# Performance work log

Hardware: AMD Instinct MI355X
Metric: run time of the kernel (lower is better)

## Reference

```python
import jax, jax.numpy as jnp
import numpy as np

TEMP = 1.0
EPS = 1e-15

B, N, F, K = 8, 2000, 128, 64


def setup_inputs() -> dict:
    key = jax.random.key(0)
    k1, k2, k3 = jax.random.split(key, 3)
    x = jax.random.normal(k1, (B, N, F), dtype=jnp.float32)
    adj = jax.random.uniform(k2, (B, N, N), dtype=jnp.float32)
    s = jax.random.normal(k3, (B, N, K), dtype=jnp.float32)
    mask = jnp.ones((B, N), dtype=bool)
    return {"x": x, "adj": adj, "s": s, "mask": mask}


def reference(x, adj, s, mask):
    k = s.shape[-1]
    s = jax.nn.softmax(s / TEMP, axis=-1)
    m = mask[..., None].astype(x.dtype)          # [B,N,1]
    x = x * m
    s = s * m

    # pooled features: s^T x -> [B,K,F]
    out = jnp.einsum('bnk,bnf->bkf', s, x)

    # pooled adjacency: s^T A s -> [B,K,K]
    as_ = jnp.einsum('bnm,bmk->bnk', adj, s)     # A s, [B,N,K]
    out_adj = jnp.einsum('bnk,bnl->bkl', as_, s)

    # mincut loss
    mincut_num = jnp.einsum('bkk->b', out_adj)
    d_flat = jnp.sum(adj, axis=-1)               # degree, [B,N]
    # trace(s^T diag(d) s) = sum_n d_n * sum_k s_nk^2 (avoids dense diag)
    mincut_den = jnp.einsum('bn,bnk,bnk->b', d_flat, s, s)
    mincut_loss = jnp.mean(-(mincut_num / mincut_den))

    # orthogonality loss
    ss = jnp.einsum('bnk,bnl->bkl', s, s)        # [B,K,K]
    ss_norm = jnp.linalg.norm(ss, axis=(-2, -1), keepdims=True)
    i_s = jnp.eye(k, dtype=ss.dtype)
    ortho = jnp.linalg.norm(ss / ss_norm - i_s / jnp.sqrt(jnp.asarray(k, ss.dtype)), axis=(-2, -1))
    ortho_loss = jnp.mean(ortho)

    # zero diagonal, symmetric degree normalization
    ind = jnp.arange(k)
    out_adj = out_adj.at[:, ind, ind].set(0.0)
    d = jnp.sqrt(jnp.sum(out_adj, axis=-1))[:, None, :] + EPS  # [B,1,K]
    out_adj = out_adj / d / jnp.swapaxes(d, 1, 2)

    return out, out_adj, mincut_loss, ortho_loss
```

## Files before the change

kernel.cpp:

```cpp
#include <hip/hip_runtime.h>

typedef __bf16 bf16;
typedef __bf16 bf16x4 __attribute__((ext_vector_type(4)));
typedef __bf16 bf16x8 __attribute__((ext_vector_type(8)));
typedef float f32x4 __attribute__((ext_vector_type(4)));

#define NB 8
#define NN 2000
#define N2 2048
#define KK 64
#define FF 128

__global__ __launch_bounds__(256) void k1_softmax(const float* __restrict__ s,
                                                  bf16* __restrict__ sT,
                                                  float* __restrict__ rowsq) {
  const int b = blockIdx.x >> 5, tile = blockIdx.x & 31;
  const int n0 = tile * 64;
  const int t = threadIdx.x;
  const int r = t >> 2, q = t & 3;
  __shared__ float ptile[64][65];
  const int n = n0 + r;
  const bool valid = n < NN;
  float v[16];
  if (valid) {
    const float4* src = (const float4*)(s + ((size_t)(b * NN + n)) * KK + q * 16);
#pragma unroll
    for (int i = 0; i < 4; ++i) {
      float4 f = src[i];
      v[4 * i + 0] = f.x; v[4 * i + 1] = f.y; v[4 * i + 2] = f.z; v[4 * i + 3] = f.w;
    }
  } else {
#pragma unroll
    for (int i = 0; i < 16; ++i) v[i] = 0.f;
  }
  float mx = v[0];
#pragma unroll
  for (int i = 1; i < 16; ++i) mx = fmaxf(mx, v[i]);
  mx = fmaxf(mx, __shfl_xor(mx, 1));
  mx = fmaxf(mx, __shfl_xor(mx, 2));
  float sum = 0.f;
#pragma unroll
  for (int i = 0; i < 16; ++i) { v[i] = __expf(v[i] - mx); sum += v[i]; }
  sum += __shfl_xor(sum, 1);
  sum += __shfl_xor(sum, 2);
  const float scale = valid ? (1.0f / sum) : 0.f;
  float rq = 0.f;
#pragma unroll
  for (int i = 0; i < 16; ++i) { v[i] *= scale; rq += v[i] * v[i]; }
  rq += __shfl_xor(rq, 1);
  rq += __shfl_xor(rq, 2);
  if (q == 0) rowsq[b * N2 + n0 + r] = rq;
#pragma unroll
  for (int i = 0; i < 16; ++i) ptile[r][q * 16 + i] = v[i];
  __syncthreads();
  bf16x8 o0, o1;
#pragma unroll
  for (int i = 0; i < 8; ++i) o0[i] = (bf16)ptile[q * 16 + i][r];
#pragma unroll
  for (int i = 0; i < 8; ++i) o1[i] = (bf16)ptile[q * 16 + 8 + i][r];
  bf16* dst = sT + ((size_t)(b * KK + r)) * N2 + n0 + q * 16;
  *(bf16x8*)dst = o0;
  *(bf16x8*)(dst + 8) = o1;
}

__global__ __launch_bounds__(256) void k2_fused(const float* __restrict__ adj,
                                                const bf16* __restrict__ sT,
                                                const float* __restrict__ x,
                                                bf16* __restrict__ xT,
                                                bf16* __restrict__ asT,
                                                const float* __restrict__ rowsq,
                                                float* __restrict__ den_part) {
  __shared__ __align__(16) float smf[64 * 132];
  const int bid = blockIdx.x;
  const int t = threadIdx.x;

  if (bid >= 1024) {
    float* xt = smf;
    const int bb = (bid - 1024) >> 5, tl = (bid - 1024) & 31;
    const int n0b = tl * 64;
#pragma unroll
    for (int i = 0; i < 8; ++i) {
      int idx = t + 256 * i;
      int row = idx >> 5, c4 = idx & 31;
      int n = n0b + row;
      float4 vv = make_float4(0.f, 0.f, 0.f, 0.f);
      if (n < NN) vv = ((const float4*)(x + ((size_t)(bb * NN + n)) * FF))[c4];
      *(float4*)&xt[row * 132 + c4 * 4] = vv;
    }
    __syncthreads();
    const int f = t >> 1, h = t & 1;
    bf16* dst = xT + ((size_t)(bb * FF + f)) * N2 + n0b + h * 32;
#pragma unroll
    for (int g = 0; g < 4; ++g) {
      bf16x8 o;
#pragma unroll
      for (int i = 0; i < 8; ++i) o[i] = (bf16)xt[(h * 32 + g * 8 + i) * 132 + f];
      *(bf16x8*)(dst + g * 8) = o;
    }
    return;
  }

  const int b = bid >> 7, tile = bid & 127;
  if (tile >= 125) {
    if (tile == 125) {
      const int k = t >> 2, seg = t & 3;
      bf16x4 z = {(bf16)0.f, (bf16)0.f, (bf16)0.f, (bf16)0.f};
      bf16* p = asT + ((size_t)(b * KK + k)) * N2 + 2000 + seg * 12;
      *(bf16x4*)(p + 0) = z; *(bf16x4*)(p + 4) = z; *(bf16x4*)(p + 8) = z;
      if (t < 3) den_part[b * 128 + 125 + t] = 0.f;
    }
    return;
  }

  const int w = t >> 6, l = t & 63;
  const int lr = l & 15, lg = l >> 4;
  const int n0 = tile * 16;
  float* dred = smf + 8192;

  const float* adjb = adj + ((size_t)(b * NN + n0)) * NN;
  const bf16* sTw = sT + ((size_t)(b * KK + w * 16 + lr)) * N2;
  const int x7 = lr & 7;

  f32x4 acc;
#pragma unroll
  for (int r = 0; r < 4; ++r) acc[r] = 0.f;

#pragma unroll
  for (int i = 0; i < 4; ++i) {
    const int rr = (w << 2) + i;
    int colf = (l ^ (rr & 7)) << 2;
    if (colf > 1996) colf = 1996;
    __builtin_amdgcn_global_load_lds(adjb + (size_t)rr * NN + colf,
                                     &smf[rr * 256], 16, 0, 0);
  }

  for (int c = 0; c < 8; ++c) {
    __syncthreads();
    if (c < 7) {
      const int nb = (c + 1) & 1;
#pragma unroll
      for (int i = 0; i < 4; ++i) {
        const int rr = (w << 2) + i;
        int colf = (c + 1) * 256 + ((l ^ (rr & 7)) << 2);
        if (colf > 1996) colf = 1996;
        __builtin_amdgcn_global_load_lds(adjb + (size_t)rr * NN + colf,
                                         &smf[nb * 4096 + rr * 256], 16, 0, 0);
      }
    }
    const float* bufc = smf + (c & 1) * 4096 + lr * 256;
    const bf16* sTc = sTw + c * 256;
#pragma unroll
    for (int st = 0; st < 8; ++st) {
      bf16x8 bfrag = *(const bf16x8*)(sTc + st * 32 + lg * 8);
      const int g0 = st * 8 + lg * 2;
      f32x4 a0 = *(const f32x4*)(bufc + ((g0 ^ x7) << 2));
      f32x4 a1 = *(const f32x4*)(bufc + (((g0 + 1) ^ x7) << 2));
      bf16x8 af;
      af[0] = (bf16)a0[0]; af[1] = (bf16)a0[1]; af[2] = (bf16)a0[2]; af[3] = (bf16)a0[3];
      af[4] = (bf16)a1[0]; af[5] = (bf16)a1[1]; af[6] = (bf16)a1[2]; af[7] = (bf16)a1[3];
      acc = __builtin_amdgcn_mfma_f32_16x16x32_bf16(af, bfrag, acc, 0, 0, 0);
    }
  }

  bf16x4 o;
#pragma unroll
  for (int r = 0; r < 4; ++r) o[r] = (bf16)acc[r];
  *(bf16x4*)(asT + ((size_t)(b * KK + w * 16 + lr)) * N2 + n0 + lg * 4) = o;

  float s0 = acc[0], s1 = acc[1], s2 = acc[2], s3 = acc[3];
#pragma unroll
  for (int off = 1; off <= 8; off <<= 1) {
    s0 += __shfl_xor(s0, off); s1 += __shfl_xor(s1, off);
    s2 += __shfl_xor(s2, off); s3 += __shfl_xor(s3, off);
  }
  const float* rqp = rowsq + b * N2 + n0 + lg * 4;
  float part = s0 * rqp[0] + s1 * rqp[1] + s2 * rqp[2] + s3 * rqp[3];
  part += __shfl_xor(part, 16);
  part += __shfl_xor(part, 32);
  if (l == 0) dred[w] = part;
  __syncthreads();
  if (t == 0) den_part[b * 128 + tile] = dred[0] + dred[1] + dred[2] + dred[3];
}

__global__ __launch_bounds__(256) void k3_gemms(const bf16* __restrict__ sT,
                                                const bf16* __restrict__ asT,
                                                const bf16* __restrict__ xT,
                                                float* __restrict__ adjraw,
                                                float* __restrict__ ssw,
                                                float* __restrict__ dout) {
  const int b = blockIdx.x >> 6, u = blockIdx.x & 63;
  const bf16 *Ab, *Bb;
  float* Cb;
  int ldC;
  if (u < 16) {
    const int rt = u >> 2, ct = u & 3;
    Ab = asT + ((size_t)(b * KK + rt * 16)) * N2;
    Bb = sT + ((size_t)(b * KK + ct * 16)) * N2;
    Cb = adjraw + b * KK * KK + rt * 16 * KK + ct * 16; ldC = KK;
  } else if (u < 32) {
    const int v = u - 16, rt = v >> 2, ct = v & 3;
    Ab = sT + ((size_t)(b * KK + rt * 16)) * N2;
    Bb = sT + ((size_t)(b * KK + ct * 16)) * N2;
    Cb = ssw + b * KK * KK + rt * 16 * KK + ct * 16; ldC = KK;
  } else {
    const int v = u - 32, rt = v >> 3, ct = v & 7;
    Ab = sT + ((size_t)(b * KK + rt * 16)) * N2;
    Bb = xT + ((size_t)(b * FF + ct * 16)) * N2;
    Cb = dout + b * KK * FF + rt * 16 * FF + ct * 16; ldC = FF;
  }
  const int t = threadIdx.x;
  const int w = t >> 6, l = t & 63;
  const int lr = l & 15, lg = l >> 4;
  f32x4 acc;
#pragma unroll
  for (int r = 0; r < 4; ++r) acc[r] = 0.f;
  const int m_begin = w * 512;
#pragma unroll 4
  for (int s = 0; s < 16; ++s) {
    const int m = m_begin + s * 32 + lg * 8;
    bf16x8 af = *(const bf16x8*)(Ab + (size_t)lr * N2 + m);
    bf16x8 bfv = *(const bf16x8*)(Bb + (size_t)lr * N2 + m);
    acc = __builtin_amdgcn_mfma_f32_16x16x32_bf16(af, bfv, acc, 0, 0, 0);
  }
  __shared__ float red[4][16][16];
#pragma unroll
  for (int r = 0; r < 4; ++r) red[w][lg * 4 + r][lr] = acc[r];
  __syncthreads();
  const int row = t >> 4, col = t & 15;
  const float v = red[0][row][col] + red[1][row][col] +
                  red[2][row][col] + red[3][row][col];
  Cb[row * ldC + col] = v;
}

__device__ inline float wred64(float v) {
#pragma unroll
  for (int off = 32; off > 0; off >>= 1) v += __shfl_xor(v, off);
  return v;
}

__global__ __launch_bounds__(64) void k4_final(const float* __restrict__ adjraw,
                                               const float* __restrict__ ssw,
                                               const float* __restrict__ den_part,
                                               float* __restrict__ dout,
                                               float* __restrict__ loss_part) {
  const int b = blockIdx.x;
  const int lane = threadIdx.x;
  const float dp = den_part[b * 128 + lane] + den_part[b * 128 + 64 + lane];
  const float den = wred64(dp);
  const float* arow = adjraw + b * 4096 + lane * 64;
  float4 av[16];
#pragma unroll
  for (int i = 0; i < 16; ++i) av[i] = ((const float4*)arow)[i];
  const float diag = adjraw[b * 4096 + lane * 65];
  float rs = 0.f;
#pragma unroll
  for (int i = 0; i < 16; ++i) rs += av[i].x + av[i].y + av[i].z + av[i].w;
  rs -= diag;
  rs = fmaxf(rs, 0.f);
  const float num = wred64(diag);
  const float d = sqrtf(rs) + 1e-15f;
  __shared__ float dsh[64];
  dsh[lane] = d;
  __syncthreads();
  const float invd = 1.0f / d;
  float* orow = dout + NB * KK * FF + b * 4096 + lane * 64;
#pragma unroll
  for (int i = 0; i < 16; ++i) {
    float4 cvv = av[i];
    cvv.x = (4 * i + 0 == lane) ? 0.f : cvv.x * invd / dsh[4 * i + 0];
    cvv.y = (4 * i + 1 == lane) ? 0.f : cvv.y * invd / dsh[4 * i + 1];
    cvv.z = (4 * i + 2 == lane) ? 0.f : cvv.z * invd / dsh[4 * i + 2];
    cvv.w = (4 * i + 3 == lane) ? 0.f : cvv.w * invd / dsh[4 * i + 3];
    ((float4*)orow)[i] = cvv;
  }
  const float* srow = ssw + b * 4096 + lane * 64;
  float4 sv[16];
  float sq = 0.f;
#pragma unroll
  for (int i = 0; i < 16; ++i) {
    sv[i] = ((const float4*)srow)[i];
    sq += sv[i].x * sv[i].x + sv[i].y * sv[i].y + sv[i].z * sv[i].z + sv[i].w * sv[i].w;
  }
  const float frob = sqrtf(wred64(sq));
  const float fi = 1.0f / frob;
  float osum = 0.f;
#pragma unroll
  for (int i = 0; i < 16; ++i) {
    float tx = sv[i].x * fi - ((4 * i + 0 == lane) ? 0.125f : 0.f);
    float ty = sv[i].y * fi - ((4 * i + 1 == lane) ? 0.125f : 0.f);
    float tz = sv[i].z * fi - ((4 * i + 2 == lane) ? 0.125f : 0.f);
    float tw = sv[i].w * fi - ((4 * i + 3 == lane) ? 0.125f : 0.f);
    osum += tx * tx + ty * ty + tz * tz + tw * tw;
  }
  const float ot = wred64(osum);
  if (lane == 0) {
    loss_part[b] = -(num / den);
    loss_part[8 + b] = sqrtf(ot);
  }
}

__global__ void k5_loss(const float* __restrict__ loss_part, float* __restrict__ dout) {
  if (threadIdx.x == 0 && blockIdx.x == 0) {
    float m = 0.f, o = 0.f;
    for (int b2 = 0; b2 < 8; ++b2) { m += loss_part[b2]; o += loss_part[8 + b2]; }
    dout[NB * KK * FF + NB * KK * KK + 0] = m * 0.125f;
    dout[NB * KK * FF + NB * KK * KK + 1] = o * 0.125f;
  }
}

extern "C" void kernel_launch(void* const* d_in, const int* in_sizes, int n_in,
                              void* d_out, int out_size, void* d_ws, size_t ws_size,
                              hipStream_t stream) {
  const float* x = (const float*)d_in[0];
  const float* adj = (const float*)d_in[1];
  const float* s = (const float*)d_in[2];
  float* out = (float*)d_out;
  char* ws = (char*)d_ws;
  bf16* sT = (bf16*)ws;
  bf16* xT = (bf16*)(ws + (2u << 20));
  bf16* asT = (bf16*)(ws + (6u << 20));
  float* rowsq = (float*)(ws + (8u << 20));
  float* den_part = (float*)(ws + (8u << 20) + 65536);
  float* adjraw = (float*)(ws + (8u << 20) + 65536 + 4096);
  float* ssw = adjraw + NB * KK * KK;
  float* loss_part = ssw + NB * KK * KK;

  k1_softmax<<<256, 256, 0, stream>>>(s, sT, rowsq);
  k2_fused<<<1280, 256, 0, stream>>>(adj, sT, x, xT, asT, rowsq, den_part);
  k3_gemms<<<512, 256, 0, stream>>>(sT, asT, xT, adjraw, ssw, out);
  k4_final<<<8, 64, 0, stream>>>(adjraw, ssw, den_part, out, loss_part);
  k5_loss<<<1, 64, 0, stream>>>(loss_part, out);
}
```

Measured before the change: 241.0 us.

## Restructure adjacency GEMM into 64-row tiles with register-staged bf16 LDS pipeline

```diff
diff --git a/kernel.cpp b/kernel.cpp
--- a/kernel.cpp
+++ b/kernel.cpp
@@ -63,24 +63,26 @@
   *(bf16x8*)(dst + 8) = o1;
 }
 
-__global__ __launch_bounds__(256) void k2_fused(const float* __restrict__ adj,
-                                                const bf16* __restrict__ sT,
-                                                const float* __restrict__ x,
-                                                bf16* __restrict__ xT,
-                                                bf16* __restrict__ asT,
-                                                const float* __restrict__ rowsq,
-                                                float* __restrict__ den_part) {
-  __shared__ __align__(16) float smf[64 * 132];
-  const int bid = blockIdx.x;
+__global__ __launch_bounds__(1024, 8) void k2_big(const float* __restrict__ adj,
+                                                  const bf16* __restrict__ sT,
+                                                  const float* __restrict__ x,
+                                                  bf16* __restrict__ xT,
+                                                  bf16* __restrict__ asT,
+                                                  const float* __restrict__ rowsq,
+                                                  float* __restrict__ den_part) {
+  __shared__ __align__(16) char smem[69632];
+  __shared__ float dredS[16];
+  const int bid0 = blockIdx.x;
   const int t = threadIdx.x;
 
-  if (bid >= 1024) {
-    float* xt = smf;
-    const int bb = (bid - 1024) >> 5, tl = (bid - 1024) & 31;
+  if (bid0 >= 256) {
+    const int lg2 = ((bid0 - 256) & 7) * 32 + ((bid0 - 256) >> 3);
+    const int bb = lg2 >> 5, tl = lg2 & 31;
     const int n0b = tl * 64;
-#pragma unroll
-    for (int i = 0; i < 8; ++i) {
-      int idx = t + 256 * i;
+    float* xt = (float*)smem;
+#pragma unroll
+    for (int i = 0; i < 2; ++i) {
+      int idx = t + 1024 * i;
       int row = idx >> 5, c4 = idx & 31;
       int n = n0b + row;
       float4 vv = make_float4(0.f, 0.f, 0.f, 0.f);
@@ -88,84 +90,88 @@
       *(float4*)&xt[row * 132 + c4 * 4] = vv;
     }
     __syncthreads();
-    const int f = t >> 1, h = t & 1;
-    bf16* dst = xT + ((size_t)(bb * FF + f)) * N2 + n0b + h * 32;
-#pragma unroll
-    for (int g = 0; g < 4; ++g) {
-      bf16x8 o;
-#pragma unroll
-      for (int i = 0; i < 8; ++i) o[i] = (bf16)xt[(h * 32 + g * 8 + i) * 132 + f];
-      *(bf16x8*)(dst + g * 8) = o;
-    }
+    const int f = t >> 3, h = t & 7;
+    bf16x8 o;
+#pragma unroll
+    for (int i = 0; i < 8; ++i) o[i] = (bf16)xt[(h * 8 + i) * 132 + f];
+    *(bf16x8*)(xT + ((size_t)(bb * FF + f)) * N2 + n0b + h * 8) = o;
     return;
   }
 
-  const int b = bid >> 7, tile = bid & 127;
-  if (tile >= 125) {
-    if (tile == 125) {
-      const int k = t >> 2, seg = t & 3;
-      bf16x4 z = {(bf16)0.f, (bf16)0.f, (bf16)0.f, (bf16)0.f};
-      bf16* p = asT + ((size_t)(b * KK + k)) * N2 + 2000 + seg * 12;
-      *(bf16x4*)(p + 0) = z; *(bf16x4*)(p + 4) = z; *(bf16x4*)(p + 8) = z;
-      if (t < 3) den_part[b * 128 + 125 + t] = 0.f;
-    }
-    return;
-  }
+  const int lgc = (bid0 & 7) * 32 + (bid0 >> 3);
+  const int b = lgc >> 5, tile = lgc & 31;
+  const int n0 = tile * 64;
 
   const int w = t >> 6, l = t & 63;
   const int lr = l & 15, lg = l >> 4;
-  const int n0 = tile * 16;
-  float* dred = smf + 8192;
-
-  const float* adjb = adj + ((size_t)(b * NN + n0)) * NN;
-  const bf16* sTw = sT + ((size_t)(b * KK + w * 16 + lr)) * N2;
-  const int x7 = lr & 7;
+  const int nr = w & 3, kr = w >> 2;
+
+  const int srow = t >> 4, scp = t & 15;
+  const bool avalid = (n0 + srow) < NN;
+  const float4* arowp = (const float4*)(adj +
+      ((size_t)(b * NN) + (avalid ? (n0 + srow) : 0)) * NN);
+  const bf16* sTrp = sT + ((size_t)(b * KK + srow)) * N2;
+
+  const int afo = (nr * 16 + lr) * 136;
+  const int bfo = 8704 + (kr * 16 + lr) * 136;
 
   f32x4 acc;
 #pragma unroll
   for (int r = 0; r < 4; ++r) acc[r] = 0.f;
 
-#pragma unroll
-  for (int i = 0; i < 4; ++i) {
-    const int rr = (w << 2) + i;
-    int colf = (l ^ (rr & 7)) << 2;
-    if (colf > 1996) colf = 1996;
-    __builtin_amdgcn_global_load_lds(adjb + (size_t)rr * NN + colf,
-                                     &smf[rr * 256], 16, 0, 0);
-  }
-
-  for (int c = 0; c < 8; ++c) {
+  float4 La0, La1;
+  bf16x8 Lb;
+
+#define K2_LOAD(C)                                                          \
+  {                                                                         \
+    const int base_ = (C) * 32 + scp * 2;                                   \
+    const int i0_ = base_ > 499 ? 499 : base_;                              \
+    const int i1_ = base_ + 1 > 499 ? 499 : base_ + 1;                      \
+    if (avalid) { La0 = arowp[i0_]; La1 = arowp[i1_]; }                     \
+    else { La0 = make_float4(0.f,0.f,0.f,0.f); La1 = La0; }                 \
+    Lb = *(const bf16x8*)(sTrp + (C) * 128 + scp * 8);                      \
+  }
+
+#define K2_WRITE(BUF)                                                       \
+  {                                                                         \
+    bf16x8 av_;                                                             \
+    av_[0] = (bf16)La0.x; av_[1] = (bf16)La0.y;                             \
+    av_[2] = (bf16)La0.z; av_[3] = (bf16)La0.w;                             \
+    av_[4] = (bf16)La1.x; av_[5] = (bf16)La1.y;                             \
+    av_[6] = (bf16)La1.z; av_[7] = (bf16)La1.w;                             \
+    bf16* p_ = (bf16*)smem + (BUF) * 17408 + srow * 136 + scp * 8;          \
+    *(bf16x8*)p_ = av_;                                                     \
+    *(bf16x8*)(p_ + 8704) = Lb;                                             \
+  }
+
+#define K2_MFMA(BUF)                                                        \
+  {                                                                         \
+    const bf16* base_ = (bf16*)smem + (BUF) * 17408;                        \
+    _Pragma("unroll")                                                       \
+    for (int ms = 0; ms < 4; ++ms) {                                        \
+      bf16x8 af_ = *(const bf16x8*)(base_ + afo + ms * 32 + lg * 8);        \
+      bf16x8 bf_ = *(const bf16x8*)(base_ + bfo + ms * 32 + lg * 8);        \
+      acc = __builtin_amdgcn_mfma_f32_16x16x32_bf16(af_, bf_, acc, 0, 0, 0);\
+    }                                                                       \
+  }
+
+  K2_LOAD(0);
+  K2_WRITE(0);
+  __syncthreads();
+  for (int c = 0; c < 16; ++c) {
+    if (c < 15) K2_LOAD(c + 1);
+    K2_MFMA(c & 1);
+    if (c < 15) K2_WRITE((c + 1) & 1);
     __syncthreads();
-    if (c < 7) {
-      const int nb = (c + 1) & 1;
-#pragma unroll
-      for (int i = 0; i < 4; ++i) {
-        const int rr = (w << 2) + i;
-        int colf = (c + 1) * 256 + ((l ^ (rr & 7)) << 2);
-        if (colf > 1996) colf = 1996;
-        __builtin_amdgcn_global_load_lds(adjb + (size_t)rr * NN + colf,
-                                         &smf[nb * 4096 + rr * 256], 16, 0, 0);
-      }
-    }
-    const float* bufc = smf + (c & 1) * 4096 + lr * 256;
-    const bf16* sTc = sTw + c * 256;
-#pragma unroll
-    for (int st = 0; st < 8; ++st) {
-      bf16x8 bfrag = *(const bf16x8*)(sTc + st * 32 + lg * 8);
-      const int g0 = st * 8 + lg * 2;
-      f32x4 a0 = *(const f32x4*)(bufc + ((g0 ^ x7) << 2));
-      f32x4 a1 = *(const f32x4*)(bufc + (((g0 + 1) ^ x7) << 2));
-      bf16x8 af;
-      af[0] = (bf16)a0[0]; af[1] = (bf16)a0[1]; af[2] = (bf16)a0[2]; af[3] = (bf16)a0[3];
-      af[4] = (bf16)a1[0]; af[5] = (bf16)a1[1]; af[6] = (bf16)a1[2]; af[7] = (bf16)a1[3];
-      acc = __builtin_amdgcn_mfma_f32_16x16x32_bf16(af, bfrag, acc, 0, 0, 0);
-    }
-  }
+  }
+#undef K2_LOAD
+#undef K2_WRITE
+#undef K2_MFMA
 
   bf16x4 o;
 #pragma unroll
   for (int r = 0; r < 4; ++r) o[r] = (bf16)acc[r];
-  *(bf16x4*)(asT + ((size_t)(b * KK + w * 16 + lr)) * N2 + n0 + lg * 4) = o;
+  *(bf16x4*)(asT + ((size_t)(b * KK + kr * 16 + lr)) * N2 + n0 + nr * 16 + lg * 4) = o;
 
   float s0 = acc[0], s1 = acc[1], s2 = acc[2], s3 = acc[3];
 #pragma unroll
@@ -173,13 +179,18 @@
     s0 += __shfl_xor(s0, off); s1 += __shfl_xor(s1, off);
     s2 += __shfl_xor(s2, off); s3 += __shfl_xor(s3, off);
   }
-  const float* rqp = rowsq + b * N2 + n0 + lg * 4;
+  const float* rqp = rowsq + b * N2 + n0 + nr * 16 + lg * 4;
   float part = s0 * rqp[0] + s1 * rqp[1] + s2 * rqp[2] + s3 * rqp[3];
   part += __shfl_xor(part, 16);
   part += __shfl_xor(part, 32);
-  if (l == 0) dred[w] = part;
-  __syncthreads();
-  if (t == 0) den_part[b * 128 + tile] = dred[0] + dred[1] + dred[2] + dred[3];
+  if (l == 0) dredS[w] = part;
+  __syncthreads();
+  if (t == 0) {
+    float dt = 0.f;
+#pragma unroll
+    for (int i = 0; i < 16; ++i) dt += dredS[i];
+    den_part[b * 32 + tile] = dt;
+  }
 }
 
 __global__ __launch_bounds__(256) void k3_gemms(const bf16* __restrict__ sT,
@@ -188,7 +199,8 @@
                                                 float* __restrict__ adjraw,
                                                 float* __restrict__ ssw,
                                                 float* __restrict__ dout) {
-  const int b = blockIdx.x >> 6, u = blockIdx.x & 63;
+  const int lgc = (blockIdx.x & 7) * 64 + (blockIdx.x >> 3);
+  const int b = lgc >> 6, u = lgc & 63;
   const bf16 *Ab, *Bb;
   float* Cb;
   int ldC;
@@ -245,7 +257,7 @@
                                                float* __restrict__ loss_part) {
   const int b = blockIdx.x;
   const int lane = threadIdx.x;
-  const float dp = den_part[b * 128 + lane] + den_part[b * 128 + 64 + lane];
+  const float dp = (lane < 32) ? den_part[b * 32 + lane] : 0.f;
   const float den = wred64(dp);
   const float* arow = adjraw + b * 4096 + lane * 64;
   float4 av[16];
@@ -326,7 +338,7 @@
   float* loss_part = ssw + NB * KK * KK;
 
   k1_softmax<<<256, 256, 0, stream>>>(s, sT, rowsq);
-  k2_fused<<<1280, 256, 0, stream>>>(adj, sT, x, xT, asT, rowsq, den_part);
+  k2_big<<<512, 1024, 0, stream>>>(adj, sT, x, xT, asT, rowsq, den_part);
   k3_gemms<<<512, 256, 0, stream>>>(sT, asT, xT, adjraw, ssw, out);
   k4_final<<<8, 64, 0, stream>>>(adjraw, ssw, den_part, out, loss_part);
   k5_loss<<<1, 64, 0, stream>>>(loss_part, out);
```

New measurement: 223.0 us. 7.5% less time.
